# Performance work log

Measured on AMD Instinct MI355X. Metric: run time of the kernel, lower is better.

## Reference

```python
import jax, jax.numpy as jnp
import numpy as np
from jax import lax

B, P, N = 32, 4096, 1024          # batch, phoneme_num, note_num
VOCAB, D, POS = 100, 256, 10      # hp.vocab_size, hp.encoder_dim, pos-emb dim
H = D                             # LSTM hidden size


def conv1d(x, w, b):
    # x: [B, Cin, L], w: [Cout, Cin, 3], padding=1 (same as torch padding=(k-1)//2)
    y = lax.conv_general_dilated(x, w, (1,), [(1, 1)], dimension_numbers=('NCH', 'OIH', 'NCH'))
    return y + b[None, :, None]


def lstm_dir(x, Wih, Whh, bih, bhh, reverse):
    # x: [B, T, I] -> [B, T, H], PyTorch gate order i,f,g,o
    Bn = x.shape[0]
    h0 = jnp.zeros((Bn, H), x.dtype)
    c0 = jnp.zeros((Bn, H), x.dtype)

    def step(carry, xt):
        h, c = carry
        z = xt @ Wih.T + h @ Whh.T + bih + bhh
        i, f, g, o = jnp.split(z, 4, axis=-1)
        c = jax.nn.sigmoid(f) * c + jax.nn.sigmoid(i) * jnp.tanh(g)
        h = jax.nn.sigmoid(o) * jnp.tanh(c)
        return (h, c), h

    _, hs = lax.scan(step, (h0, c0), x.transpose(1, 0, 2), reverse=reverse)
    return hs.transpose(1, 0, 2)


def bilstm(x, wih, whh, bih, bhh):
    f = lstm_dir(x, wih[0], whh[0], bih[0], bhh[0], False)
    b = lstm_dir(x, wih[1], whh[1], bih[1], bhh[1], True)
    return jnp.concatenate([f, b], axis=-1)


def _forward(score_note_dur, phoneme_seq, phoneme_order, emb, pos_emb,
             mix_w1, mix_b1, mix_w2, mix_b2,
             wih0, whh0, bih0, bhh0, wih1, whh1, bih1, bhh1,
             cnn_w1, cnn_b1, cnn_w2, cnn_b2):
    pe = emb[phoneme_seq]            # [B,P,D]
    po = pos_emb[phoneme_order]      # [B,P,10]
    x = jnp.concatenate([pe, po], axis=-1).transpose(0, 2, 1)  # [B,D+10,P]
    x = jax.nn.relu(conv1d(x, mix_w1, mix_b1))
    x = conv1d(x, mix_w2, mix_b2).transpose(0, 2, 1)            # [B,P,D]

    # Vectorized version of the nested note-boundary loop:
    # runs of tokens > 1 map, in order, to notes 0,1,2,...; the last position is
    # never included (torch loop stops at phoneme_end < len-1 and slices [start:end)).
    Lp = phoneme_seq.shape[1]
    valid = phoneme_seq > 1
    valid = valid.at[:, Lp - 1].set(False)
    prev = jnp.pad(valid[:, :-1], ((0, 0), (1, 0)))
    starts = valid & ~prev
    seg = jnp.cumsum(starts.astype(jnp.int32), axis=1) - 1
    seg = jnp.where(valid, seg, N)  # separators / overflow -> dump segment N

    def agg_one(xb, sb):
        s = jax.ops.segment_sum(xb, sb, num_segments=N + 1)
        c = jax.ops.segment_sum(jnp.ones((Lp,), xb.dtype), sb, num_segments=N + 1)
        return s[:N] / jnp.maximum(c[:N, None], 1.0)

    agg = jax.vmap(agg_one)(x, seg)  # [B,N,D]; empty notes stay zero

    d = score_note_dur[..., None]
    enc = jnp.concatenate([agg, d, 1.0 / (d + 1.0)], axis=-1)  # [B,N,D+2]
    y = bilstm(enc, wih0, whh0, bih0, bhh0)
    y = bilstm(y, wih1, whh1, bih1, bhh1)                       # [B,N,2H]
    y = y.transpose(0, 2, 1)
    y = jax.nn.relu(conv1d(y, cnn_w1, cnn_b1))
    y = conv1d(y, cnn_w2, cnn_b2)
    return y.transpose(0, 2, 1)  # [B,N,1]


def setup_inputs() -> dict:
    keys = iter(jax.random.split(jax.random.key(0), 24))

    def nrm(shape, scale):
        return jax.random.normal(next(keys), shape, jnp.float32) * scale

    s = 1.0 / float(np.sqrt(H))
    inp = {}
    inp['score_note_dur'] = jax.random.uniform(next(keys), (B, N), jnp.float32) * 4.0
    inp['phoneme_seq'] = jax.random.randint(next(keys), (B, P), 0, 8)
    inp['phoneme_order'] = jax.random.randint(next(keys), (B, P), 0, 20)
    inp['emb'] = nrm((VOCAB, D), 0.1).at[0].set(0.0)       # padding_idx=0
    inp['pos_emb'] = nrm((20, POS), 0.1).at[0].set(0.0)    # padding_idx=0
    inp['mix_w1'] = nrm((D, D + POS, 3), s)
    inp['mix_b1'] = jnp.zeros((D,), jnp.float32)
    inp['mix_w2'] = nrm((D, D, 3), s)
    inp['mix_b2'] = jnp.zeros((D,), jnp.float32)
    inp['wih0'] = nrm((2, 4 * H, D + 2), s)
    inp['whh0'] = nrm((2, 4 * H, H), s)
    inp['bih0'] = jnp.zeros((2, 4 * H), jnp.float32)
    inp['bhh0'] = jnp.zeros((2, 4 * H), jnp.float32)
    inp['wih1'] = nrm((2, 4 * H, 2 * H), s)
    inp['whh1'] = nrm((2, 4 * H, H), s)
    inp['bih1'] = jnp.zeros((2, 4 * H), jnp.float32)
    inp['bhh1'] = jnp.zeros((2, 4 * H), jnp.float32)
    inp['cnn_w1'] = nrm((D, 2 * H, 3), s)
    inp['cnn_b1'] = jnp.zeros((D,), jnp.float32)
    inp['cnn_w2'] = nrm((1, D, 3), s)
    inp['cnn_b2'] = jnp.zeros((1,), jnp.float32)
    return inp


def reference(score_note_dur, phoneme_seq, phoneme_order, emb, pos_emb,
              mix_w1, mix_b1, mix_w2, mix_b2,
              wih0, whh0, bih0, bhh0, wih1, whh1, bih1, bhh1,
              cnn_w1, cnn_b1, cnn_w2, cnn_b2):
    return _forward(score_note_dur, phoneme_seq, phoneme_order, emb, pos_emb,
                    mix_w1, mix_b1, mix_w2, mix_b2,
                    wih0, whh0, bih0, bhh0, wih1, whh1, bih1, bhh1,
                    cnn_w1, cnn_b1, cnn_w2, cnn_b2)
```

## Files before the change

### kernel.cpp

```cpp
#include <hip/hip_runtime.h>
#include <math.h>

#define B_    32
#define P_    4096
#define N_    1024
#define POS_  10
#define PP    (P_ + 2)
#define NP    (N_ + 2)
#define GB    8
#define NCHK  (B_ / GB)
#define TCH   128
#define NTCH  (N_ / TCH)
#define X0S   280
#define ENCS  288
#define LROW  80
#define LTILE (64 * LROW)
#define GEMM_LDS (3 * LTILE)

typedef unsigned short u16;
typedef _Float16 h2_t __attribute__((ext_vector_type(2)));
typedef unsigned u32x4 __attribute__((ext_vector_type(4)));
typedef short s16x8 __attribute__((ext_vector_type(8)));
typedef float f32x4 __attribute__((ext_vector_type(4)));

__device__ __forceinline__ float sigmoidf_(float x) { return 1.f / (1.f + __expf(-x)); }
__device__ __forceinline__ float tanhf_(float x) {
  float t = fminf(fmaxf(x, -30.f), 30.f);
  float e = __expf(2.f * t);
  return (e - 1.f) / (e + 1.f);
}
__device__ __forceinline__ float bf2f(u16 u) { return __uint_as_float(((unsigned)u) << 16); }
__device__ __forceinline__ u16 f2bf(float f) {
  unsigned u = __float_as_uint(f);
  unsigned r = u + 0x7FFFu + ((u >> 16) & 1u);
  return (u16)(r >> 16);
}
__device__ __forceinline__ u16 f2h_bits(float x) {
  _Float16 hh = (_Float16)x; u16 u; __builtin_memcpy(&u, &hh, 2); return u;
}
__device__ __forceinline__ unsigned pack2h(float lo, float hi) {
  return (unsigned)f2h_bits(lo) | ((unsigned)f2h_bits(hi) << 16);
}
__device__ __forceinline__ float dot2(unsigned w, unsigned h, float acc) {
  return __builtin_amdgcn_fdot2(__builtin_bit_cast(h2_t, w), __builtin_bit_cast(h2_t, h), acc, false);
}
#define DOT4(acc, wq, hq) \
  acc = dot2((wq).x, (hq).x, acc); acc = dot2((wq).y, (hq).y, acc); \
  acc = dot2((wq).z, (hq).z, acc); acc = dot2((wq).w, (hq).w, acc);

#define REP24(X) X(0)X(1)X(2)X(3)X(4)X(5)X(6)X(7)X(8)X(9)X(10)X(11)X(12)X(13)X(14)X(15)X(16)X(17)X(18)X(19)X(20)X(21)X(22)X(23)
#define REP8(X)  X(0)X(1)X(2)X(3)X(4)X(5)X(6)X(7)

__device__ __forceinline__ void stc(float* p, float v) { *p = v; }
__device__ __forceinline__ void stc(u16* p, float v)   { *p = f2bf(v); }

__global__ void fill_sentinel_kernel(float* out, int n, float v) {
  int i = blockIdx.x * 256 + threadIdx.x;
  if (i < n) out[i] = v;
}

__global__ void zero_bf_guards_kernel(u16* X0b, u16* X1b) {
  int cb = blockIdx.x, t = threadIdx.x;
  for (int c = t; c < X0S; c += 256) {
    X0b[((long)cb * PP + 0) * X0S + c] = 0;
    X0b[((long)cb * PP + PP - 1) * X0S + c] = 0;
  }
  if (t < 256) {
    X1b[((long)cb * PP + 0) * 256 + t] = 0;
    X1b[((long)cb * PP + PP - 1) * 256 + t] = 0;
  }
}
__global__ void zero_y1p_guards_kernel(u16* Y1p) {
  int b = blockIdx.x, t = threadIdx.x;
  for (int c = t; c < 512; c += 256) {
    Y1p[((long)b * NP + 0) * 512 + c] = 0;
    Y1p[((long)b * NP + NP - 1) * 512 + c] = 0;
  }
}
__global__ void zero_c3p_guards_kernel(float* C3p) {
  int b = blockIdx.x, t = threadIdx.x;
  if (t < 256) {
    C3p[((long)b * NP + 0) * 256 + t] = 0.f;
    C3p[((long)b * NP + NP - 1) * 256 + t] = 0.f;
  }
}

__global__ void embed_bf16_kernel(const int* __restrict__ seq, const int* __restrict__ order,
                                  const float* __restrict__ emb, const float* __restrict__ pos_emb,
                                  u16* __restrict__ X0b, int b0) {
  long i = (long)blockIdx.x * 256 + threadIdx.x;
  const long total = (long)GB * P_ * X0S;
  if (i >= total) return;
  int c = (int)(i % X0S);
  long bp = i / X0S;
  int p = (int)(bp % P_);
  int cb = (int)(bp / P_);
  int b = b0 + cb;
  float v = 0.f;
  if (c < 256)      v = emb[(long)seq[(long)b * P_ + p] * 256 + c];
  else if (c < 266) v = pos_emb[(long)order[(long)b * P_ + p] * POS_ + (c - 256)];
  X0b[((long)cb * PP + p + 1) * X0S + c] = f2bf(v);
}

__global__ void repack_conv_bt_kernel(const float* __restrict__ w, u16* __restrict__ hi,
                                      u16* __restrict__ lo, int CinReal, int strideA,
                                      int Kpad, int Cout) {
  long i = (long)blockIdx.x * 256 + threadIdx.x;
  if (i >= (long)Cout * Kpad) return;
  int co = (int)(i / Kpad), k = (int)(i - (long)co * Kpad);
  int r = k / strideA, ci = k - r * strideA;
  float v = (r < 3 && ci < CinReal) ? w[((long)co * CinReal + ci) * 3 + r] : 0.f;
  u16 h = f2bf(v);
  hi[i] = h;
  if (lo) lo[i] = f2bf(v - bf2f(h));
}
__global__ void repack_dense_bt_kernel(const float* __restrict__ w, u16* __restrict__ hi,
                                       u16* __restrict__ lo, int CinReal, int Kpad) {
  long i = (long)blockIdx.x * 256 + threadIdx.x;
  if (i >= 1024L * Kpad) return;
  int j = (int)(i / Kpad), k = (int)(i - (long)j * Kpad);
  int co = (j & 3) * 256 + (j >> 2);
  float v = (k < CinReal) ? w[(long)co * CinReal + k] : 0.f;
  u16 h = f2bf(v);
  hi[i] = h;
  lo[i] = f2bf(v - bf2f(h));
}
__global__ void repack_whh_reg_kernel(const float* __restrict__ whh, uint4* __restrict__ Wv) {
  long i = (long)blockIdx.x * 256 + threadIdx.x;
  if (i >= 49152) return;
  int j = (int)(i & 511);
  int t = (int)(i >> 9);
  int kq = t % 24, rb = (t / 24) & 1, d = t / 48;
  int R = (j & 3) * 256 + (j >> 2) + rb * 128;
  const float* wr = whh + ((long)d * 1024 + R) * 256;
  uint4 o; unsigned* op = (unsigned*)&o;
#pragma unroll
  for (int q = 0; q < 4; q++) {
    int k = kq * 8 + 2 * q;
    op[q] = pack2h(wr[k], wr[k + 1]);
  }
  Wv[i] = o;
}
__global__ void repack_whh_lds_kernel(const float* __restrict__ whh, uint4* __restrict__ Ws) {
  long i = (long)blockIdx.x * 256 + threadIdx.x;
  if (i >= 16384) return;
  int d = (int)(i >> 13);
  int a = (int)(i & 8191);
  int rb = a >> 12;
  int rem = a & 4095;
  int i2 = rem >> 9, j = rem & 511;
  int R = (j & 3) * 256 + (j >> 2) + rb * 128;
  const float* wr = whh + ((long)d * 1024 + R) * 256;
  uint4 o; unsigned* op = (unsigned*)&o;
#pragma unroll
  for (int q = 0; q < 4; q++) {
    int k = 192 + i2 * 8 + 2 * q;
    op[q] = pack2h(wr[k], wr[k + 1]);
  }
  Ws[i] = o;
}
__global__ void bias_sum_perm_kernel(const float* __restrict__ a, const float* __restrict__ b,
                                     float* __restrict__ dst) {
  int i = blockIdx.x * 256 + threadIdx.x;
  if (i >= 2048) return;
  int d = i >> 10, j = i & 1023;
  int R = (j & 3) * 256 + (j >> 2);
  dst[i] = a[d * 1024 + R] + b[d * 1024 + R];
}
__global__ void repack_conv4_w_kernel(const float* __restrict__ w, float* __restrict__ dst) {
  int i = blockIdx.x * 256 + threadIdx.x;
  if (i < 768) { int r = i >> 8, ci = i & 255; dst[i] = w[ci * 3 + r]; }
}

template <typename CT, bool SPLIT>
__device__ __forceinline__ void gemm_tile_lds(
    char* smbase, int tid, int bx, int by,
    const u16* __restrict__ A, const u16* __restrict__ Bt, const u16* __restrict__ Bt2,
    const float* __restrict__ bias, CT* __restrict__ C,
    int N, int Kpad, int Mb,
    long aBatchStride, int aRowStride,
    long cBatchStride, int cRowStride, int relu) {
  char* As = smbase;
  char* Bh = smbase + LTILE;
  char* Bl = smbase + 2 * LTILE;
  int wave = tid >> 6, lane = tid & 63;
  int lrow = lane & 15, lkg = lane >> 4;
  int row0 = bx * 64, col0 = by * 64;
  int srow = tid >> 2, skoff = (tid & 3) * 8;
  int sgrow = row0 + srow;
  int sb = sgrow / Mb, smr = sgrow - sb * Mb;
  const u16* gA  = A + (long)sb * aBatchStride + (long)smr * aRowStride + skoff;
  const u16* gBh = Bt + (long)(col0 + srow) * Kpad + skoff;
  const u16* gBl = SPLIT ? (Bt2 + (long)(col0 + srow) * Kpad + skoff) : gBh;
  int wb = srow * LROW + (tid & 3) * 16;
  int frow = wave * 16 + lrow;
  int ab  = frow * LROW + lkg * 16;
  int bb0 = lrow * LROW + lkg * 16;

  f32x4 acc0 = {0.f, 0.f, 0.f, 0.f};
  f32x4 acc1 = acc0, acc2 = acc0, acc3 = acc0;
  for (int kk = 0; kk < Kpad; kk += 32) {
    s16x8 ra  = *(const s16x8*)(gA + kk);
    s16x8 rbh = *(const s16x8*)(gBh + kk);
    s16x8 rbl;
    if (SPLIT) rbl = *(const s16x8*)(gBl + kk);
    __syncthreads();
    *(s16x8*)(As + wb) = ra;
    *(s16x8*)(Bh + wb) = rbh;
    if (SPLIT) *(s16x8*)(Bl + wb) = rbl;
    __syncthreads();
    s16x8 av = *(const s16x8*)(As + ab);
    acc0 = __builtin_amdgcn_mfma_f32_16x16x32_bf16(av, *(const s16x8*)(Bh + bb0 + 0 * (16 * LROW)), acc0, 0, 0, 0);
    acc1 = __builtin_amdgcn_mfma_f32_16x16x32_bf16(av, *(const s16x8*)(Bh + bb0 + 1 * (16 * LROW)), acc1, 0, 0, 0);
    acc2 = __builtin_amdgcn_mfma_f32_16x16x32_bf16(av, *(const s16x8*)(Bh + bb0 + 2 * (16 * LROW)), acc2, 0, 0, 0);
    acc3 = __builtin_amdgcn_mfma_f32_16x16x32_bf16(av, *(const s16x8*)(Bh + bb0 + 3 * (16 * LROW)), acc3, 0, 0, 0);
    if (SPLIT) {
      acc0 = __builtin_amdgcn_mfma_f32_16x16x32_bf16(av, *(const s16x8*)(Bl + bb0 + 0 * (16 * LROW)), acc0, 0, 0, 0);
      acc1 = __builtin_amdgcn_mfma_f32_16x16x32_bf16(av, *(const s16x8*)(Bl + bb0 + 1 * (16 * LROW)), acc1, 0, 0, 0);
      acc2 = __builtin_amdgcn_mfma_f32_16x16x32_bf16(av, *(const s16x8*)(Bl + bb0 + 2 * (16 * LROW)), acc2, 0, 0, 0);
      acc3 = __builtin_amdgcn_mfma_f32_16x16x32_bf16(av, *(const s16x8*)(Bl + bb0 + 3 * (16 * LROW)), acc3, 0, 0, 0);
    }
  }
  int erow = row0 + wave * 16 + lkg * 4;
  int b2 = erow / Mb, m2 = erow - b2 * Mb;
  CT* cbase = C + (long)b2 * cBatchStride + (long)m2 * cRowStride + col0 + lrow;
#define EPI(cc, accv) { \
    float bv = bias[col0 + (cc) * 16 + lrow]; \
    float v0 = accv[0] + bv, v1 = accv[1] + bv, v2 = accv[2] + bv, v3 = accv[3] + bv; \
    if (relu) { v0 = fmaxf(v0, 0.f); v1 = fmaxf(v1, 0.f); v2 = fmaxf(v2, 0.f); v3 = fmaxf(v3, 0.f); } \
    stc(cbase + 0L * cRowStride + (cc) * 16, v0); \
    stc(cbase + 1L * cRowStride + (cc) * 16, v1); \
    stc(cbase + 2L * cRowStride + (cc) * 16, v2); \
    stc(cbase + 3L * cRowStride + (cc) * 16, v3); }
  EPI(0, acc0) EPI(1, acc1) EPI(2, acc2) EPI(3, acc3)
#undef EPI
}

template <typename CT, bool SPLIT>
__global__ __launch_bounds__(256) void gemm_mfma_kernel(
    const u16* __restrict__ A, const u16* __restrict__ Bt, const u16* __restrict__ Bt2,
    const float* __restrict__ bias, CT* __restrict__ C,
    int N, int Kpad, int Mb,
    long aBatchStride, int aRowStride,
    long cBatchStride, int cRowStride, int relu) {
  __shared__ char smtile[GEMM_LDS];
  gemm_tile_lds<CT, SPLIT>(smtile, threadIdx.x, blockIdx.x, blockIdx.y,
                           A, Bt, Bt2, bias, C, N, Kpad, Mb,
                           aBatchStride, aRowStride, cBatchStride, cRowStride, relu);
}

__global__ __launch_bounds__(256) void seg_scan_kernel(const int* __restrict__ seq,
                                int* __restrict__ nstart, int* __restrict__ nlen) {
  __shared__ unsigned char v[P_];
  __shared__ int sc[2][256];
  int b = blockIdx.x, tid = threadIdx.x;
  for (int i = tid; i < P_; i += 256) {
    int s = seq[(long)b * P_ + i];
    v[i] = (s > 1 && i != P_ - 1) ? 1 : 0;
  }
  for (int n = tid; n < N_; n += 256) { nstart[b * N_ + n] = 0; nlen[b * N_ + n] = 0; }
  __syncthreads();
  int base = tid << 4;
  int c = 0;
#pragma unroll
  for (int i = 0; i < 16; i++) {
    int p = base + i;
    int val = v[p];
    int prev = p ? v[p - 1] : 0;
    c += val & (prev ^ 1);
  }
  sc[0][tid] = c;
  __syncthreads();
  int cur = 0;
  for (int d = 1; d < 256; d <<= 1) {
    int x = sc[cur][tid];
    if (tid >= d) x += sc[cur][tid - d];
    sc[cur ^ 1][tid] = x;
    cur ^= 1;
    __syncthreads();
  }
  int sg = tid ? sc[cur][tid - 1] : 0;
  for (int i = 0; i < 16; i++) {
    int p = base + i;
    int val = v[p];
    int prev = p ? v[p - 1] : 0;
    if (val && !prev) {
      if (sg < N_) {
        int len = 0, q = p;
        while (q < P_ && v[q]) { len++; q++; }
        nstart[b * N_ + sg] = p;
        nlen[b * N_ + sg] = len;
      }
      sg++;
    }
  }
}

__global__ __launch_bounds__(256) void agg_enc_kernel(
    const u16* __restrict__ X2b, const int* __restrict__ nstart, const int* __restrict__ nlen,
    const float* __restrict__ dur, u16* __restrict__ enc, int b0) {
  int n = blockIdx.x, gb = blockIdx.y;
  int b = b0 + gb;
  int d = threadIdx.x;
  int len = nlen[b * N_ + n], st = nstart[b * N_ + n];
  float acc = 0.f;
  for (int i = 0; i < len; i++) acc += bf2f(X2b[((long)gb * PP + st + 1 + i) * 256 + d]);
  float m = (len > 0) ? acc / (float)len : 0.f;
  long e = ((long)b * N_ + n) * ENCS;
  enc[e + d] = f2bf(m);
  if (d == 0) {
    float dd = dur[b * N_ + n];
    enc[e + 256] = f2bf(dd);
    enc[e + 257] = f2bf(1.f / (dd + 1.f));
  }
  if (d >= 2 && d < 32) enc[e + 256 + d] = 0;
}

#define REC_LDS_BYTES (131072 + 4096 + 1024)
__global__ __attribute__((amdgpu_waves_per_eu(2, 2))) __launch_bounds__(512)
void rec_gemm_kernel(
    const float* __restrict__ Z,
    const u32x4* __restrict__ Wv,
    const u32x4* __restrict__ Ws,
    float* __restrict__ state,
    u16* __restrict__ Y, int yRowsPerB, int yPad, int r,
    const u16* __restrict__ Xg, const u16* __restrict__ Whg, const u16* __restrict__ Wlg,
    const float* __restrict__ bsg, float* __restrict__ Zg, int Kpg, int rq) {
  extern __shared__ char smem[];
  int tid = threadIdx.x;
  if (blockIdx.x >= 64) {
    int half = tid >> 8, vt = tid & 255;
    int tile = (blockIdx.x - 64) * 2 + half;
    int dir = tile >> 10;
    int t2 = tile & 1023;
    int bx = t2 & 63, by = t2 >> 6;
    int t0g = (dir == 0) ? rq * TCH : (NTCH - 1 - rq) * TCH;
    long WihD = (long)1024 * Kpg;
    long ZD = (long)B_ * TCH * 1024;
    gemm_tile_lds<float, true>(smem + half * GEMM_LDS, vt, bx, by,
        Xg + (long)t0g * Kpg, Whg + (long)dir * WihD, Wlg + (long)dir * WihD,
        bsg + dir * 1024, Zg + (long)dir * ZD,
        1024, Kpg, TCH, (long)N_ * Kpg, Kpg, (long)TCH * 1024, 1024, 0);
    return;
  }
  u32x4* WL = (u32x4*)smem;
  float* zb = (float*)(smem + 131072);
  u16*   hb = (u16*)(smem + 131072 + 4096);
  const u32x4* hb4 = (const u32x4*)hb;

  int chain = blockIdx.x;
  int d = chain >> 5, b = chain & 31;
  const float* Zb = Z + (long)(d * 32 + b) * (TCH * 1024);

  for (int iq = 0; iq < 16; ++iq) {
    int q = iq * 512 + tid;
    WL[q] = Ws[(long)d * 8192 + q];
  }
  const u32x4* WvD = Wv + (long)d * 2 * 24 * 512;
#define DECLW(i) u32x4 wA##i, wB##i;
  REP24(DECLW)
#undef DECLW
#define LOADW(i) wA##i = WvD[(i) * 512 + tid]; wB##i = WvD[(24 + (i)) * 512 + tid];
  REP24(LOADW)
#undef LOADW
#define PINW(i) asm volatile("" : "+v"(wA##i), "+v"(wB##i));
  REP24(PINW)
#undef PINW

  float h_reg = 0.f, c_reg = 0.f;
  if (tid < 256) {
    if (r > 0) {
      h_reg = state[(chain * 2 + 0) * 256 + tid];
      c_reg = state[(chain * 2 + 1) * 256 + tid];
    }
    hb[tid] = f2h_bits(h_reg);
  }
  __syncthreads();

  int t0 = (d == 0) ? r * TCH : (NTCH - 1 - r) * TCH;
  int tcf = d ? (TCH - 1) : 0;
  float preA = Zb[(long)tcf * 1024 + tid];
  float preB = Zb[(long)tcf * 1024 + 512 + tid];

  for (int tt = 0; tt < TCH; ++tt) {
    float accA = preA, accB = preB;
    if (tt + 1 < TCH) {
      int tc2 = d ? (TCH - 2 - tt) : (tt + 1);
      preA = Zb[(long)tc2 * 1024 + tid];
      preB = Zb[(long)tc2 * 1024 + 512 + tid];
    }
#define MACW(i) { u32x4 hq = hb4[i]; DOT4(accA, wA##i, hq); DOT4(accB, wB##i, hq); }
    REP24(MACW)
#undef MACW
#define MACL(i) { u32x4 hq = hb4[24 + (i)]; \
                  u32x4 qa = WL[(i) * 512 + tid]; \
                  u32x4 qb = WL[4096 + (i) * 512 + tid]; \
                  DOT4(accA, qa, hq); DOT4(accB, qb, hq); }
    REP8(MACL)
#undef MACL
    zb[tid] = accA;
    zb[tid + 512] = accB;
    __syncthreads();
    int tcur = d ? (TCH - 1 - tt) : tt;
    if (tid < 256) {
      float4 z4 = *(const float4*)&zb[tid * 4];
      float ig = sigmoidf_(z4.x), fg = sigmoidf_(z4.y);
      float gg = tanhf_(z4.z), og = sigmoidf_(z4.w);
      c_reg = fg * c_reg + ig * gg;
      float h = og * tanhf_(c_reg);
      h_reg = h;
      hb[tid] = f2h_bits(h);
      Y[((long)b * yRowsPerB + t0 + tcur + yPad) * 512 + d * 256 + tid] = f2bf(h);
    }
    __syncthreads();
  }
  if (r != NTCH - 1 && tid < 256) {
    state[(chain * 2 + 0) * 256 + tid] = h_reg;
    state[(chain * 2 + 1) * 256 + tid] = c_reg;
  }
}

__global__ __launch_bounds__(256) void conv4_kernel(
    const float* __restrict__ C3p, const float* __restrict__ w,
    const float* __restrict__ b2, float* __restrict__ out) {
  int row = blockIdx.x * 4 + (threadIdx.x >> 6);
  int lane = threadIdx.x & 63;
  int b = row >> 10, t = row & (N_ - 1);
  const float* a = C3p + ((long)b * NP + t) * 256;
  float acc = 0.f;
  for (int k = lane; k < 768; k += 64) acc += a[k] * w[k];
  for (int off = 32; off; off >>= 1) acc += __shfl_down(acc, off, 64);
  if (lane == 0) out[row] = acc + b2[0];
}

extern "C" void kernel_launch(void* const* d_in, const int* in_sizes, int n_in,
                              void* d_out, int out_size, void* d_ws, size_t ws_size,
                              hipStream_t stream) {
  const float* dur     = (const float*)d_in[0];
  const int*   seq     = (const int*)d_in[1];
  const int*   order   = (const int*)d_in[2];
  const float* emb     = (const float*)d_in[3];
  const float* pos_emb = (const float*)d_in[4];
  const float* mix_w1  = (const float*)d_in[5];
  const float* mix_b1  = (const float*)d_in[6];
  const float* mix_w2  = (const float*)d_in[7];
  const float* mix_b2  = (const float*)d_in[8];
  const float* wih0    = (const float*)d_in[9];
  const float* whh0    = (const float*)d_in[10];
  const float* bih0    = (const float*)d_in[11];
  const float* bhh0    = (const float*)d_in[12];
  const float* wih1    = (const float*)d_in[13];
  const float* whh1    = (const float*)d_in[14];
  const float* bih1    = (const float*)d_in[15];
  const float* bhh1    = (const float*)d_in[16];
  const float* cnn_w1  = (const float*)d_in[17];
  const float* cnn_b1  = (const float*)d_in[18];
  const float* cnn_w2  = (const float*)d_in[19];
  const float* cnn_b2  = (const float*)d_in[20];
  float* out = (float*)d_out;
  float* ws = (float*)d_ws;

  (void)hipFuncSetAttribute((const void*)rec_gemm_kernel,
                            hipFuncAttributeMaxDynamicSharedMemorySize, REC_LDS_BYTES);

  const long X0B_F = (long)GB * PP * X0S / 2;
  const long X1B_F = (long)GB * PP * 256 / 2;
  const long X2B_F = X1B_F;
  const long ZE2   = 2L * B_ * TCH * 1024;
  const long C3P_E = (long)B_ * NP * 256;
  long region = X0B_F + X1B_F + X2B_F;
  if (2 * ZE2 > region) region = 2 * ZE2;
  if (C3P_E > region) region = C3P_E;

  long off = 0;
  auto alloc = [&](long n) { long ret = off; off += (n + 15) & ~15L; return ret; };
  long o_region = alloc(region);
  long o_enc    = alloc((long)B_ * N_ * ENCS / 2);
  long o_Y0     = alloc((long)B_ * N_ * 512 / 2);
  long o_Y1p    = alloc((long)B_ * NP * 512 / 2);
  long o_W1h    = alloc(256L * 832 / 2);
  long o_W2h    = alloc(256L * 768 / 2);
  long o_Wc1h   = alloc(256L * 1536 / 2);
  long o_Wc1l   = alloc(256L * 1536 / 2);
  long o_Wc2r   = alloc(768);
  long o_Wih0h  = alloc(2L * 1024 * ENCS / 2);
  long o_Wih0l  = alloc(2L * 1024 * ENCS / 2);
  long o_Wih1h  = alloc(2L * 1024 * 512 / 2);
  long o_Wih1l  = alloc(2L * 1024 * 512 / 2);
  long o_Wv0    = alloc(49152L * 4);
  long o_Ws0    = alloc(16384L * 4);
  long o_Wv1    = alloc(49152L * 4);
  long o_Ws1    = alloc(16384L * 4);
  long o_bs0    = alloc(2048);
  long o_bs1    = alloc(2048);
  long o_state  = alloc(64L * 2 * 256);
  long o_nst    = alloc((long)B_ * N_);
  long o_nln    = alloc((long)B_ * N_);

  if ((size_t)(off * 4) > ws_size) {
    float v = -(1000.0f + (float)(ws_size >> 20));
    fill_sentinel_kernel<<<(out_size + 255) / 256, 256, 0, stream>>>(out, out_size, v);
    return;
  }

  u16*   X0b  = (u16*)(ws + o_region);
  u16*   X1b  = (u16*)(ws + o_region + X0B_F);
  u16*   X2b  = (u16*)(ws + o_region + X0B_F + X1B_F);
  float* Zbuf[2] = { ws + o_region, ws + o_region + ZE2 };
  float* C3p  = ws + o_region;
  u16*   enc  = (u16*)(ws + o_enc);
  u16*   Y0   = (u16*)(ws + o_Y0);
  u16*   Y1p  = (u16*)(ws + o_Y1p);
  u16*   W1h  = (u16*)(ws + o_W1h);
  u16*   W2h  = (u16*)(ws + o_W2h);
  u16*   Wc1h = (u16*)(ws + o_Wc1h);
  u16*   Wc1l = (u16*)(ws + o_Wc1l);
  float* Wc2r = ws + o_Wc2r;
  u16*   Wih0h = (u16*)(ws + o_Wih0h);
  u16*   Wih0l = (u16*)(ws + o_Wih0l);
  u16*   Wih1h = (u16*)(ws + o_Wih1h);
  u16*   Wih1l = (u16*)(ws + o_Wih1l);
  uint4* Wv0  = (uint4*)(ws + o_Wv0);
  uint4* Ws0  = (uint4*)(ws + o_Ws0);
  uint4* Wv1  = (uint4*)(ws + o_Wv1);
  uint4* Ws1  = (uint4*)(ws + o_Ws1);
  float* bs0  = ws + o_bs0;
  float* bs1  = ws + o_bs1;
  float* state = ws + o_state;
  int* nstart = (int*)(ws + o_nst);
  int* nlen   = (int*)(ws + o_nln);

  zero_bf_guards_kernel<<<GB, 256, 0, stream>>>(X0b, X1b);
  zero_y1p_guards_kernel<<<B_, 256, 0, stream>>>(Y1p);
  repack_conv_bt_kernel<<<(int)((256L * 832 + 255) / 256), 256, 0, stream>>>(
      mix_w1, W1h, nullptr, 266, X0S, 832, 256);
  repack_conv_bt_kernel<<<(int)((256L * 768 + 255) / 256), 256, 0, stream>>>(
      mix_w2, W2h, nullptr, 256, 256, 768, 256);
  repack_conv_bt_kernel<<<(int)((256L * 1536 + 255) / 256), 256, 0, stream>>>(
      cnn_w1, Wc1h, Wc1l, 512, 512, 1536, 256);
  repack_conv4_w_kernel<<<3, 256, 0, stream>>>(cnn_w2, Wc2r);
  for (int d = 0; d < 2; d++) {
    repack_dense_bt_kernel<<<(int)((1024L * ENCS + 255) / 256), 256, 0, stream>>>(
        wih0 + (long)d * 1024 * 258, Wih0h + (long)d * 1024 * ENCS,
        Wih0l + (long)d * 1024 * ENCS, 258, ENCS);
    repack_dense_bt_kernel<<<(int)((1024L * 512 + 255) / 256), 256, 0, stream>>>(
        wih1 + (long)d * 1024 * 512, Wih1h + (long)d * 1024 * 512,
        Wih1l + (long)d * 1024 * 512, 512, 512);
  }
  repack_whh_reg_kernel<<<192, 256, 0, stream>>>(whh0, Wv0);
  repack_whh_lds_kernel<<<64, 256, 0, stream>>>(whh0, Ws0);
  repack_whh_reg_kernel<<<192, 256, 0, stream>>>(whh1, Wv1);
  repack_whh_lds_kernel<<<64, 256, 0, stream>>>(whh1, Ws1);
  bias_sum_perm_kernel<<<8, 256, 0, stream>>>(bih0, bhh0, bs0);
  bias_sum_perm_kernel<<<8, 256, 0, stream>>>(bih1, bhh1, bs1);
  seg_scan_kernel<<<B_, 256, 0, stream>>>(seq, nstart, nlen);

  for (int ch = 0; ch < NCHK; ch++) {
    int b0 = ch * GB;
    long total = (long)GB * P_ * X0S;
    embed_bf16_kernel<<<(int)((total + 255) / 256), 256, 0, stream>>>(seq, order, emb, pos_emb, X0b, b0);
    gemm_mfma_kernel<u16, false><<<dim3(GB * P_ / 64, 4), 256, 0, stream>>>(
        X0b, W1h, nullptr, mix_b1, X1b + 256,
        256, 832, P_, (long)PP * X0S, X0S, (long)PP * 256, 256, 1);
    gemm_mfma_kernel<u16, false><<<dim3(GB * P_ / 64, 4), 256, 0, stream>>>(
        X1b, W2h, nullptr, mix_b2, X2b + 256,
        256, 768, P_, (long)PP * 256, 256, (long)PP * 256, 256, 0);
    agg_enc_kernel<<<dim3(N_, GB), 256, 0, stream>>>(X2b, nstart, nlen, dur, enc, b0);
  }

  const long ZD = (long)B_ * TCH * 1024;
  for (int layer = 0; layer < 2; layer++) {
    const u16*  Xl   = (layer == 0) ? enc : Y0;
    int         Kp   = (layer == 0) ? ENCS : 512;
    const u16*  Wh   = (layer == 0) ? Wih0h : Wih1h;
    const u16*  Wl   = (layer == 0) ? Wih0l : Wih1l;
    long        WihD = (long)1024 * Kp;
    const float* bsl = (layer == 0) ? bs0 : bs1;
    const u32x4* Wv  = (const u32x4*)((layer == 0) ? Wv0 : Wv1);
    const u32x4* Wsp = (const u32x4*)((layer == 0) ? Ws0 : Ws1);
    u16*        Yl   = (layer == 0) ? Y0 : Y1p;
    int         yRows = (layer == 0) ? N_ : NP;
    int         yPad  = (layer == 0) ? 0 : 1;
    for (int d = 0; d < 2; d++) {
      int t0 = (d == 0) ? 0 : (NTCH - 1) * TCH;
      gemm_mfma_kernel<float, true><<<dim3(B_ * TCH / 64, 16), 256, 0, stream>>>(
          Xl + (long)t0 * Kp, Wh + (long)d * WihD, Wl + (long)d * WihD,
          bsl + d * 1024, Zbuf[0] + d * ZD,
          1024, Kp, TCH, (long)N_ * Kp, Kp, (long)TCH * 1024, 1024, 0);
    }
    for (int r = 0; r < NTCH; r++) {
      int gemmWGs = (r < NTCH - 1) ? 1024 : 0;
      rec_gemm_kernel<<<64 + gemmWGs, 512, REC_LDS_BYTES, stream>>>(
          Zbuf[r & 1], Wv, Wsp, state, Yl, yRows, yPad, r,
          Xl, Wh, Wl, bsl, Zbuf[(r + 1) & 1], Kp, r + 1);
    }
  }

  zero_c3p_guards_kernel<<<B_, 256, 0, stream>>>(C3p);
  gemm_mfma_kernel<float, true><<<dim3(B_ * N_ / 64, 4), 256, 0, stream>>>(
      Y1p, Wc1h, Wc1l, cnn_b1, C3p + 256,
      256, 1536, N_, (long)NP * 512, 512, (long)NP * 256, 256, 1);
  conv4_kernel<<<B_ * N_ / 4, 256, 0, stream>>>(C3p, Wc2r, cnn_b2, out);
}
```

Before: 4.421 ms.

## Use 1024-thread recurrent blocks with one gate row per thread

The recurrent LSTM kernel now runs 1024 threads per chain, with each thread owning one gate row instead of two. Register-held weights drop to 24 uint4 per thread and the dot products are split across four independent accumulators to shorten dependency chains. The gate repack kernels are reindexed to match, and the fused input-GEMM blocks now handle four tiles per block instead of two. The aim is lower per-step latency on the serial recurrence. The cost is more threads per barrier, and each GEMM-side block now needs four GEMM_LDS regions (at least 61440 bytes), which the launch at REC_LDS_BYTES and the recurrent smem layout must still cover.

```diff
diff --git a/kernel.cpp b/kernel.cpp
--- a/kernel.cpp
+++ b/kernel.cpp
@@ -44,12 +44,8 @@
 __device__ __forceinline__ float dot2(unsigned w, unsigned h, float acc) {
   return __builtin_amdgcn_fdot2(__builtin_bit_cast(h2_t, w), __builtin_bit_cast(h2_t, h), acc, false);
 }
-#define DOT4(acc, wq, hq) \
-  acc = dot2((wq).x, (hq).x, acc); acc = dot2((wq).y, (hq).y, acc); \
-  acc = dot2((wq).z, (hq).z, acc); acc = dot2((wq).w, (hq).w, acc);
 
 #define REP24(X) X(0)X(1)X(2)X(3)X(4)X(5)X(6)X(7)X(8)X(9)X(10)X(11)X(12)X(13)X(14)X(15)X(16)X(17)X(18)X(19)X(20)X(21)X(22)X(23)
-#define REP8(X)  X(0)X(1)X(2)X(3)X(4)X(5)X(6)X(7)
 
 __device__ __forceinline__ void stc(float* p, float v) { *p = v; }
 __device__ __forceinline__ void stc(u16* p, float v)   { *p = f2bf(v); }
@@ -128,10 +124,10 @@
 __global__ void repack_whh_reg_kernel(const float* __restrict__ whh, uint4* __restrict__ Wv) {
   long i = (long)blockIdx.x * 256 + threadIdx.x;
   if (i >= 49152) return;
-  int j = (int)(i & 511);
-  int t = (int)(i >> 9);
-  int kq = t % 24, rb = (t / 24) & 1, d = t / 48;
-  int R = (j & 3) * 256 + (j >> 2) + rb * 128;
+  int j = (int)(i & 1023);
+  int t = (int)(i >> 10);
+  int kq = t % 24, d = t / 24;
+  int R = (j & 3) * 256 + (j >> 2);
   const float* wr = whh + ((long)d * 1024 + R) * 256;
   uint4 o; unsigned* op = (unsigned*)&o;
 #pragma unroll
@@ -144,12 +140,10 @@
 __global__ void repack_whh_lds_kernel(const float* __restrict__ whh, uint4* __restrict__ Ws) {
   long i = (long)blockIdx.x * 256 + threadIdx.x;
   if (i >= 16384) return;
-  int d = (int)(i >> 13);
-  int a = (int)(i & 8191);
-  int rb = a >> 12;
-  int rem = a & 4095;
-  int i2 = rem >> 9, j = rem & 511;
-  int R = (j & 3) * 256 + (j >> 2) + rb * 128;
+  int j = (int)(i & 1023);
+  int t = (int)(i >> 10);
+  int i2 = t & 7, d = t >> 3;
+  int R = (j & 3) * 256 + (j >> 2);
   const float* wr = whh + ((long)d * 1024 + R) * 256;
   uint4 o; unsigned* op = (unsigned*)&o;
 #pragma unroll
@@ -317,7 +311,7 @@
 }
 
 #define REC_LDS_BYTES (131072 + 4096 + 1024)
-__global__ __attribute__((amdgpu_waves_per_eu(2, 2))) __launch_bounds__(512)
+__global__ __launch_bounds__(1024)
 void rec_gemm_kernel(
     const float* __restrict__ Z,
     const u32x4* __restrict__ Wv,
@@ -329,15 +323,15 @@
   extern __shared__ char smem[];
   int tid = threadIdx.x;
   if (blockIdx.x >= 64) {
-    int half = tid >> 8, vt = tid & 255;
-    int tile = (blockIdx.x - 64) * 2 + half;
+    int quarter = tid >> 8, vt = tid & 255;
+    int tile = (blockIdx.x - 64) * 4 + quarter;
     int dir = tile >> 10;
     int t2 = tile & 1023;
     int bx = t2 & 63, by = t2 >> 6;
     int t0g = (dir == 0) ? rq * TCH : (NTCH - 1 - rq) * TCH;
     long WihD = (long)1024 * Kpg;
     long ZD = (long)B_ * TCH * 1024;
-    gemm_tile_lds<float, true>(smem + half * GEMM_LDS, vt, bx, by,
+    gemm_tile_lds<float, true>(smem + quarter * GEMM_LDS, vt, bx, by,
         Xg + (long)t0g * Kpg, Whg + (long)dir * WihD, Wlg + (long)dir * WihD,
         bsg + dir * 1024, Zg + (long)dir * ZD,
         1024, Kpg, TCH, (long)N_ * Kpg, Kpg, (long)TCH * 1024, 1024, 0);
@@ -352,18 +346,18 @@
   int d = chain >> 5, b = chain & 31;
   const float* Zb = Z + (long)(d * 32 + b) * (TCH * 1024);
 
-  for (int iq = 0; iq < 16; ++iq) {
-    int q = iq * 512 + tid;
+  for (int iq = 0; iq < 8; ++iq) {
+    int q = iq * 1024 + tid;
     WL[q] = Ws[(long)d * 8192 + q];
   }
-  const u32x4* WvD = Wv + (long)d * 2 * 24 * 512;
-#define DECLW(i) u32x4 wA##i, wB##i;
+  const u32x4* WvD = Wv + (long)d * 24 * 1024;
+#define DECLW(i) u32x4 wq##i;
   REP24(DECLW)
 #undef DECLW
-#define LOADW(i) wA##i = WvD[(i) * 512 + tid]; wB##i = WvD[(24 + (i)) * 512 + tid];
+#define LOADW(i) wq##i = WvD[(long)(i) * 1024 + tid];
   REP24(LOADW)
 #undef LOADW
-#define PINW(i) asm volatile("" : "+v"(wA##i), "+v"(wB##i));
+#define PINW(i) asm volatile("" : "+v"(wq##i));
   REP24(PINW)
 #undef PINW
 
@@ -379,27 +373,32 @@
 
   int t0 = (d == 0) ? r * TCH : (NTCH - 1 - r) * TCH;
   int tcf = d ? (TCH - 1) : 0;
-  float preA = Zb[(long)tcf * 1024 + tid];
-  float preB = Zb[(long)tcf * 1024 + 512 + tid];
+  float pre = Zb[(long)tcf * 1024 + tid];
 
   for (int tt = 0; tt < TCH; ++tt) {
-    float accA = preA, accB = preB;
+    float acc0 = pre, acc1 = 0.f, acc2 = 0.f, acc3 = 0.f;
     if (tt + 1 < TCH) {
       int tc2 = d ? (TCH - 2 - tt) : (tt + 1);
-      preA = Zb[(long)tc2 * 1024 + tid];
-      preB = Zb[(long)tc2 * 1024 + 512 + tid];
+      pre = Zb[(long)tc2 * 1024 + tid];
     }
-#define MACW(i) { u32x4 hq = hb4[i]; DOT4(accA, wA##i, hq); DOT4(accB, wB##i, hq); }
-    REP24(MACW)
+#define MACW(i, a) { u32x4 hq = hb4[i]; \
+  acc##a = dot2(wq##i.x, hq.x, acc##a); acc##a = dot2(wq##i.y, hq.y, acc##a); \
+  acc##a = dot2(wq##i.z, hq.z, acc##a); acc##a = dot2(wq##i.w, hq.w, acc##a); }
+    MACW(0,0) MACW(1,1) MACW(2,2) MACW(3,3)
+    MACW(4,0) MACW(5,1) MACW(6,2) MACW(7,3)
+    MACW(8,0) MACW(9,1) MACW(10,2) MACW(11,3)
+    MACW(12,0) MACW(13,1) MACW(14,2) MACW(15,3)
+    MACW(16,0) MACW(17,1) MACW(18,2) MACW(19,3)
+    MACW(20,0) MACW(21,1) MACW(22,2) MACW(23,3)
 #undef MACW
-#define MACL(i) { u32x4 hq = hb4[24 + (i)]; \
-                  u32x4 qa = WL[(i) * 512 + tid]; \
-                  u32x4 qb = WL[4096 + (i) * 512 + tid]; \
-                  DOT4(accA, qa, hq); DOT4(accB, qb, hq); }
-    REP8(MACL)
+#define MACL(i, a) { u32x4 hq = hb4[24 + (i)]; \
+  u32x4 q = WL[(long)(i) * 1024 + tid]; \
+  acc##a = dot2(q.x, hq.x, acc##a); acc##a = dot2(q.y, hq.y, acc##a); \
+  acc##a = dot2(q.z, hq.z, acc##a); acc##a = dot2(q.w, hq.w, acc##a); }
+    MACL(0,0) MACL(1,1) MACL(2,2) MACL(3,3)
+    MACL(4,0) MACL(5,1) MACL(6,2) MACL(7,3)
 #undef MACL
-    zb[tid] = accA;
-    zb[tid + 512] = accB;
+    zb[tid] = (acc0 + acc2) + (acc1 + acc3);
     __syncthreads();
     int tcur = d ? (TCH - 1 - tt) : tt;
     if (tid < 256) {
@@ -589,8 +588,8 @@
           1024, Kp, TCH, (long)N_ * Kp, Kp, (long)TCH * 1024, 1024, 0);
     }
     for (int r = 0; r < NTCH; r++) {
-      int gemmWGs = (r < NTCH - 1) ? 1024 : 0;
-      rec_gemm_kernel<<<64 + gemmWGs, 512, REC_LDS_BYTES, stream>>>(
+      int gemmWGs = (r < NTCH - 1) ? 512 : 0;
+      rec_gemm_kernel<<<64 + gemmWGs, 1024, REC_LDS_BYTES, stream>>>(
           Zbuf[r & 1], Wv, Wsp, state, Yl, yRows, yPad, r,
           Xl, Wh, Wl, bsl, Zbuf[(r + 1) & 1], Kp, r + 1);
     }
```

After: 8.686 ms. +96.5%, slower.

## Exchange LSTM gates via DPP quad permutes and double-buffer hidden state

Applied to the files above, without the earlier changes.

The LSTM recurrent step used to write all gate pre-activations to LDS, synchronize, and let 256 threads compute the cell update. Now every thread applies its own activation, the four gates of a unit are gathered within a quad using DPP permutes, and each quad computes the cell update redundantly. The hidden-state buffer is double-buffered, which removes one __syncthreads per timestep. This relies on gate rows being interleaved so each quad holds i,f,g,o for the same unit, and it adds redundant transcendental work across lanes.

```diff
diff --git a/kernel.cpp b/kernel.cpp
--- a/kernel.cpp
+++ b/kernel.cpp
@@ -50,6 +50,9 @@
 
 #define REP24(X) X(0)X(1)X(2)X(3)X(4)X(5)X(6)X(7)X(8)X(9)X(10)X(11)X(12)X(13)X(14)X(15)X(16)X(17)X(18)X(19)X(20)X(21)X(22)X(23)
 #define REP8(X)  X(0)X(1)X(2)X(3)X(4)X(5)X(6)X(7)
+
+#define QPERM(dst, v, ctrl) \
+  dst = __int_as_float(__builtin_amdgcn_update_dpp(0, __float_as_int(v), (ctrl), 0xf, 0xf, true));
 
 __device__ __forceinline__ void stc(float* p, float v) { *p = v; }
 __device__ __forceinline__ void stc(u16* p, float v)   { *p = f2bf(v); }
@@ -344,9 +347,7 @@
     return;
   }
   u32x4* WL = (u32x4*)smem;
-  float* zb = (float*)(smem + 131072);
   u16*   hb = (u16*)(smem + 131072 + 4096);
-  const u32x4* hb4 = (const u32x4*)hb;
 
   int chain = blockIdx.x;
   int d = chain >> 5, b = chain & 31;
@@ -367,13 +368,21 @@
   REP24(PINW)
 #undef PINW
 
-  float h_reg = 0.f, c_reg = 0.f;
-  if (tid < 256) {
-    if (r > 0) {
-      h_reg = state[(chain * 2 + 0) * 256 + tid];
-      c_reg = state[(chain * 2 + 1) * 256 + tid];
-    }
-    hb[tid] = f2h_bits(h_reg);
+  int g = tid & 3;
+  int u = tid >> 2;
+  bool isG = (g == 2);
+  bool lead = (g == 0);
+
+  float hA = 0.f, cA = 0.f, hB = 0.f, cB = 0.f;
+  if (r > 0) {
+    hA = state[(chain * 2 + 0) * 256 + u];
+    cA = state[(chain * 2 + 1) * 256 + u];
+    hB = state[(chain * 2 + 0) * 256 + u + 128];
+    cB = state[(chain * 2 + 1) * 256 + u + 128];
+  }
+  if (lead) {
+    hb[u] = f2h_bits(hA);
+    hb[u + 128] = f2h_bits(hB);
   }
   __syncthreads();
 
@@ -383,6 +392,8 @@
   float preB = Zb[(long)tcf * 1024 + 512 + tid];
 
   for (int tt = 0; tt < TCH; ++tt) {
+    int cur = tt & 1;
+    const u32x4* hb4 = (const u32x4*)(hb + cur * 256);
     float accA = preA, accB = preB;
     if (tt + 1 < TCH) {
       int tc2 = d ? (TCH - 2 - tt) : (tt + 1);
@@ -398,25 +409,44 @@
                   DOT4(accA, qa, hq); DOT4(accB, qb, hq); }
     REP8(MACL)
 #undef MACL
-    zb[tid] = accA;
-    zb[tid + 512] = accB;
-    __syncthreads();
+    float vA = isG ? tanhf_(accA) : sigmoidf_(accA);
+    float vB = isG ? tanhf_(accB) : sigmoidf_(accB);
+    float a1, a2, a3, b1, b2, b3;
+    QPERM(a1, vA, 0xB1)
+    QPERM(a2, vA, 0x4E)
+    QPERM(a3, vA, 0x1B)
+    QPERM(b1, vB, 0xB1)
+    QPERM(b2, vB, 0x4E)
+    QPERM(b3, vB, 0x1B)
+    bool lo = (tid & 1), hi = (tid & 2);
+    float iA = hi ? (lo ? a3 : a2) : (lo ? a1 : vA);
+    float fA = hi ? (lo ? a2 : a3) : (lo ? vA : a1);
+    float gA = hi ? (lo ? a1 : vA) : (lo ? a3 : a2);
+    float oA = hi ? (lo ? vA : a1) : (lo ? a2 : a3);
+    float iB = hi ? (lo ? b3 : b2) : (lo ? b1 : vB);
+    float fB = hi ? (lo ? b2 : b3) : (lo ? vB : b1);
+    float gB = hi ? (lo ? b1 : vB) : (lo ? b3 : b2);
+    float oB = hi ? (lo ? vB : b1) : (lo ? b2 : b3);
+    cA = fA * cA + iA * gA;
+    hA = oA * tanhf_(cA);
+    cB = fB * cB + iB * gB;
+    hB = oB * tanhf_(cB);
     int tcur = d ? (TCH - 1 - tt) : tt;
-    if (tid < 256) {
-      float4 z4 = *(const float4*)&zb[tid * 4];
-      float ig = sigmoidf_(z4.x), fg = sigmoidf_(z4.y);
-      float gg = tanhf_(z4.z), og = sigmoidf_(z4.w);
-      c_reg = fg * c_reg + ig * gg;
-      float h = og * tanhf_(c_reg);
-      h_reg = h;
-      hb[tid] = f2h_bits(h);
-      Y[((long)b * yRowsPerB + t0 + tcur + yPad) * 512 + d * 256 + tid] = f2bf(h);
+    if (lead) {
+      u16* hbn = hb + ((cur ^ 1) * 256);
+      hbn[u] = f2h_bits(hA);
+      hbn[u + 128] = f2h_bits(hB);
+      long yb = ((long)b * yRowsPerB + t0 + tcur + yPad) * 512 + d * 256;
+      Y[yb + u] = f2bf(hA);
+      Y[yb + u + 128] = f2bf(hB);
     }
     __syncthreads();
   }
-  if (r != NTCH - 1 && tid < 256) {
-    state[(chain * 2 + 0) * 256 + tid] = h_reg;
-    state[(chain * 2 + 1) * 256 + tid] = c_reg;
+  if (r != NTCH - 1 && lead) {
+    state[(chain * 2 + 0) * 256 + u] = hA;
+    state[(chain * 2 + 1) * 256 + u] = cA;
+    state[(chain * 2 + 0) * 256 + u + 128] = hB;
+    state[(chain * 2 + 1) * 256 + u + 128] = cB;
   }
 }
 
```

Result: slower. 16.53 ms (+274.0%).
